# Performance work log

Measured on AMD Instinct MI355X. Metric: run time of the kernel, lower is better.

## Reference

```python
import jax, jax.numpy as jnp
import numpy as np

B, S_IMG, S_TXT = 2, 2048, 256
DIM, H, D = 1024, 16, 64
EPS = 1e-6


def _rmsnorm(x, w):
    x32 = x.astype(jnp.float32)
    rms = jnp.sqrt(jnp.mean(x32 * x32, axis=-1, keepdims=True) + EPS)
    return (x32 / rms * w.astype(jnp.float32)).astype(x.dtype)


def _heads(x):  # [B,S,DIM] -> [B,H,S,D]
    b, s, _ = x.shape
    return x.reshape(b, s, H, D).transpose(0, 2, 1, 3)


def setup_inputs() -> dict:
    key = jax.random.key(0)
    ks = jax.random.split(key, 20)
    lin = lambda k: (jax.random.normal(k, (DIM, DIM), jnp.float32) * 0.02,
                     jnp.zeros((DIM,), jnp.float32))
    wq, bq = lin(ks[0]); wk, bk = lin(ks[1]); wv, bv = lin(ks[2])
    waq, baq = lin(ks[3]); wak, bak = lin(ks[4]); wav, bav = lin(ks[5])
    wout, bout = lin(ks[6]); waout, baout = lin(ks[7])
    return {
        "img_hidden": jax.random.normal(ks[8], (B, S_IMG, DIM), jnp.float32),
        "txt_hidden": jax.random.normal(ks[9], (B, S_TXT, DIM), jnp.float32),
        "wq": wq, "bq": bq, "wk": wk, "bk": bk, "wv": wv, "bv": bv,
        "waq": waq, "baq": baq, "wak": wak, "bak": bak, "wav": wav, "bav": bav,
        "wout": wout, "bout": bout, "waout": waout, "baout": baout,
        "gq": jnp.ones((D,), jnp.float32), "gk": jnp.ones((D,), jnp.float32),
        "gaq": jnp.ones((D,), jnp.float32), "gak": jnp.ones((D,), jnp.float32),
    }


def reference(img_hidden, txt_hidden, wq, bq, wk, bk, wv, bv,
              waq, baq, wak, bak, wav, bav, wout, bout, waout, baout,
              gq, gk, gaq, gak):
    batch = img_hidden.shape[0]
    # joint QKV projections (torch Linear: x @ W.T + b)
    q = _heads(img_hidden @ wq.T + bq)
    k = _heads(img_hidden @ wk.T + bk)
    v = _heads(img_hidden @ wv.T + bv)
    aq = _heads(txt_hidden @ waq.T + baq)
    ak = _heads(txt_hidden @ wak.T + bak)
    av = _heads(txt_hidden @ wav.T + bav)
    # per-head RMSNorm on Q/K
    q, k = _rmsnorm(q, gq), _rmsnorm(k, gk)
    aq, ak = _rmsnorm(aq, gaq), _rmsnorm(ak, gak)
    # concat streams along sequence: [B,H,S_img+S_txt,D]
    fq = jnp.concatenate([q, aq], axis=2)
    fk = jnp.concatenate([k, ak], axis=2)
    fv = jnp.concatenate([v, av], axis=2)
    scale = 1.0 / jnp.sqrt(jnp.float32(D))
    attn = jnp.einsum('bhqd,bhkd->bhqk', fq, fk) * scale
    attn = jax.nn.softmax(attn, axis=-1)
    out = jnp.einsum('bhqk,bhkd->bhqd', attn, fv)
    out = out.transpose(0, 2, 1, 3)  # [B,S,H,D]
    s_img = q.shape[2]
    img_out = out[:, :s_img].reshape(batch, s_img, -1)
    txt_out = out[:, s_img:].reshape(batch, aq.shape[2], -1)
    img_out = img_out @ wout.T + bout
    txt_out = txt_out @ waout.T + baout
    return (img_out, txt_out)
```

## Files before the change

kernel.cpp:

```cpp
#include <hip/hip_runtime.h>
#include <stdint.h>

#define BATCH 2
#define SIMG 2048
#define STXT 256
#define STOT 2304
#define DIM 1024
#define NH 16
#define HD 64

typedef unsigned short u16;
typedef __attribute__((ext_vector_type(8))) short bf16x8;
typedef __attribute__((ext_vector_type(4))) float f32x4;

__device__ __forceinline__ u16 f2bf(float f) {
  union { float f; uint32_t u; } v; v.f = f;
  uint32_t r = (v.u + 0x7FFFu + ((v.u >> 16) & 1u)) >> 16;
  return (u16)r;
}
__device__ __forceinline__ float bf2f(u16 h) {
  union { uint32_t u; float f; } v; v.u = ((uint32_t)h) << 16; return v.f;
}

__device__ __forceinline__ void async_load16(const u16* g, u16* l) {
  __builtin_amdgcn_global_load_lds(
      (const __attribute__((address_space(1))) uint32_t*)g,
      (__attribute__((address_space(3))) uint32_t*)l, 16, 0, 0);
}

__device__ __forceinline__ bf16x8 cvt8(const float* p) {
  const f32x4 a = *(const f32x4*)p;
  const f32x4 b = *(const f32x4*)(p + 4);
  union { bf16x8 v; u16 s[8]; } r;
  r.s[0] = f2bf(a[0]); r.s[1] = f2bf(a[1]); r.s[2] = f2bf(a[2]); r.s[3] = f2bf(a[3]);
  r.s[4] = f2bf(b[0]); r.s[5] = f2bf(b[1]); r.s[6] = f2bf(b[2]); r.s[7] = f2bf(b[3]);
  return r.v;
}

__device__ __forceinline__ float gain_at(const u16* g, int d) {
  if (g[0] == 0) return ((const float*)g)[d];
  return bf2f(g[d]);
}

__global__ __launch_bounds__(256)
void cvt_all(const float* s0, const float* s1, const float* s2, const float* s3,
             const float* s4, const float* s5, const float* s6, const float* s7,
             const float* s8, const float* s9,
             u16* d0, u16* d1, u16* d2, u16* d3, u16* d4,
             u16* d5, u16* d6, u16* d7, u16* d8, u16* d9)
{
  const int z = blockIdx.z;
  const float* srcs[10] = {s0,s1,s2,s3,s4,s5,s6,s7,s8,s9};
  u16* dsts[10] = {d0,d1,d2,d3,d4,d5,d6,d7,d8,d9};
  const int ns[10] = {BATCH*SIMG*DIM, BATCH*STXT*DIM, DIM*DIM, DIM*DIM, DIM*DIM,
                      DIM*DIM, DIM*DIM, DIM*DIM, DIM*DIM, DIM*DIM};
  const long i = ((long)blockIdx.x * 256 + threadIdx.x) * 8;
  if (i >= ns[z]) return;
  *(bf16x8*)(dsts[z] + i) = cvt8(srcs[z] + i);
}

template<int MODE>
__global__ __launch_bounds__(256)
void gemm_bt(const u16* __restrict__ Ai, const u16* __restrict__ At,
             const u16* __restrict__ Wi0, const u16* __restrict__ Wi1, const u16* __restrict__ Wi2,
             const u16* __restrict__ Wt0, const u16* __restrict__ Wt1, const u16* __restrict__ Wt2,
             const float* __restrict__ bi0, const float* __restrict__ bi1, const float* __restrict__ bi2,
             const float* __restrict__ bt0, const float* __restrict__ bt1, const float* __restrict__ bt2,
             void* __restrict__ Di0, void* __restrict__ Di1, void* __restrict__ Di2,
             void* __restrict__ Dt0, void* __restrict__ Dt1, void* __restrict__ Dt2,
             const u16* __restrict__ gi0, const u16* __restrict__ gi1,
             const u16* __restrict__ gt0, const u16* __restrict__ gt1,
             int ysplit)
{
  const int z = blockIdx.z;
  const bool txt = (int)blockIdx.y >= ysplit;
  const int yy = txt ? ((int)blockIdx.y - ysplit) : (int)blockIdx.y;

  const u16* A = txt ? At : Ai;
  const u16* W      = txt ? ((z == 0) ? Wt0 : ((z == 1) ? Wt1 : Wt2))
                          : ((z == 0) ? Wi0 : ((z == 1) ? Wi1 : Wi2));
  const float* bias = txt ? ((z == 0) ? bt0 : ((z == 1) ? bt1 : bt2))
                          : ((z == 0) ? bi0 : ((z == 1) ? bi1 : bi2));
  void* Dst         = txt ? ((z == 0) ? Dt0 : ((z == 1) ? Dt1 : Dt2))
                          : ((z == 0) ? Di0 : ((z == 1) ? Di1 : Di2));

  const int slog = txt ? 8 : 11;
  const int smask = (1 << slog) - 1;
  const int batch_rows = (MODE == 0) ? (txt ? STXT : SIMG) : STOT;
  const int src_off    = (MODE == 0) ? 0 : (txt ? SIMG : 0);
  const int dst_off    = (MODE == 0) ? (txt ? SIMG : 0) : 0;

  const int m0 = yy * 128;
  const int n0 = blockIdx.x * 128;
  const int tid = threadIdx.x;
  const int lane = tid & 63;
  const int w = tid >> 6;
  const int wm = w >> 1, wn = w & 1;
  const int l15 = lane & 15, quad = lane >> 4;

  __shared__ __attribute__((aligned(16))) u16 As[128 * 32];
  __shared__ __attribute__((aligned(16))) u16 Bs[128 * 32];

  const int srow = tid >> 2;
  const int scol = (tid & 3) * 8;

  long aoff0, aoff1;
  {
    int m = m0 + srow;
    aoff0 = ((long)(m >> slog) * batch_rows + src_off + (m & smask)) * DIM + scol;
    m = m0 + 64 + srow;
    aoff1 = ((long)(m >> slog) * batch_rows + src_off + (m & smask)) * DIM + scol;
  }
  const u16* wp0 = W + (long)(n0 + srow) * DIM + scol;
  const u16* wp1 = W + (long)(n0 + 64 + srow) * DIM + scol;
  u16* as0 = As + tid * 8;
  u16* as1 = As + 2048 + tid * 8;
  u16* bs0 = Bs + tid * 8;
  u16* bs1 = Bs + 2048 + tid * 8;

  const f32x4 fzero = {0.f, 0.f, 0.f, 0.f};
  f32x4 acc[4][4];
  #pragma unroll
  for (int i = 0; i < 4; ++i)
    #pragma unroll
    for (int j = 0; j < 4; ++j) acc[i][j] = fzero;

  for (int kt = 0; kt < DIM; kt += 32) {
    __syncthreads();
    async_load16(A + aoff0 + kt, as0);
    async_load16(A + aoff1 + kt, as1);
    async_load16(wp0 + kt, bs0);
    async_load16(wp1 + kt, bs1);
    __syncthreads();

    bf16x8 af[4], bfg[4];
    #pragma unroll
    for (int mt = 0; mt < 4; ++mt)
      af[mt] = *(const bf16x8*)(As + (wm * 64 + mt * 16 + l15) * 32 + quad * 8);
    #pragma unroll
    for (int nt = 0; nt < 4; ++nt)
      bfg[nt] = *(const bf16x8*)(Bs + (wn * 64 + nt * 16 + l15) * 32 + quad * 8);
    #pragma unroll
    for (int mt = 0; mt < 4; ++mt)
      #pragma unroll
      for (int nt = 0; nt < 4; ++nt)
        acc[mt][nt] = __builtin_amdgcn_mfma_f32_16x16x32_bf16(af[mt], bfg[nt], acc[mt][nt], 0, 0, 0);
  }

  if (MODE == 0 && z != 2) {
    const u16* gsel = txt ? ((z == 0) ? gt0 : gt1) : ((z == 0) ? gi0 : gi1);
    float gv[4];
    #pragma unroll
    for (int nt = 0; nt < 4; ++nt) gv[nt] = gain_at(gsel, nt * 16 + l15);
    #pragma unroll
    for (int mt = 0; mt < 4; ++mt) {
      float vals[4][4];
      #pragma unroll
      for (int nt = 0; nt < 4; ++nt) {
        const float bb = bias[n0 + wn * 64 + nt * 16 + l15];
        #pragma unroll
        for (int r = 0; r < 4; ++r) vals[nt][r] = acc[mt][nt][r] + bb;
      }
      #pragma unroll
      for (int r = 0; r < 4; ++r) {
        float ss = vals[0][r] * vals[0][r] + vals[1][r] * vals[1][r]
                 + vals[2][r] * vals[2][r] + vals[3][r] * vals[3][r];
        #pragma unroll
        for (int d = 1; d < 16; d <<= 1) ss += __shfl_xor(ss, d, 64);
        const float scn = rsqrtf(ss * (1.0f / 64.0f) + 1e-6f);
        const int grow = m0 + wm * 64 + mt * 16 + quad * 4 + r;
        const int b = grow >> slog;
        const int sl = grow & smask;
        #pragma unroll
        for (int nt = 0; nt < 4; ++nt) {
          const int gcol = n0 + wn * 64 + nt * 16 + l15;
          const int h = gcol >> 6, d2 = gcol & 63;
          const long idx = (((long)(b * NH + h)) * STOT + dst_off + sl) * HD + d2;
          ((u16*)Dst)[idx] = f2bf(vals[nt][r] * scn * gv[nt]);
        }
      }
    }
  } else {
    #pragma unroll
    for (int mt = 0; mt < 4; ++mt) {
      #pragma unroll
      for (int nt = 0; nt < 4; ++nt) {
        const int gcol = n0 + wn * 64 + nt * 16 + l15;
        const float bb = bias[gcol];
        const f32x4 v = acc[mt][nt];
        #pragma unroll
        for (int r = 0; r < 4; ++r) {
          const int grow = m0 + wm * 64 + mt * 16 + quad * 4 + r;
          const float val = v[r] + bb;
          if (MODE == 0) {
            const int b = grow >> slog;
            const int sl = grow & smask;
            const int h = gcol >> 6, d = gcol & 63;
            const long idx = (((long)(b * NH + h)) * HD + d) * STOT + dst_off + sl;
            ((u16*)Dst)[idx] = f2bf(val);
          } else {
            ((float*)Dst)[(long)grow * DIM + gcol] = val;
          }
        }
      }
    }
  }
}

__global__ __launch_bounds__(256)
void flash_attn(const u16* __restrict__ fq, const u16* __restrict__ fk,
                const u16* __restrict__ fvT, u16* __restrict__ aout)
{
  const int qt = blockIdx.x;
  const int bh = blockIdx.y;
  const int tid = threadIdx.x;
  const int lane = tid & 63;
  const int w = tid >> 6;
  const int l15 = lane & 15, quad = lane >> 4;
  const int x7 = l15 & 7;
  const long base = (long)bh * STOT * HD;
  const int b = bh >> 4, h = bh & 15;

  __shared__ __attribute__((aligned(16))) u16 Ks[64 * 64];
  __shared__ __attribute__((aligned(16))) u16 Vt[64 * 64];
  __shared__ __attribute__((aligned(16))) u16 Ps[64 * 72];

  bf16x8 aq[2];
  #pragma unroll
  for (int ks = 0; ks < 2; ++ks)
    aq[ks] = *(const bf16x8*)(fq + base +
        (long)(qt * 64 + w * 16 + l15) * 64 + ks * 32 + quad * 8);

  const f32x4 fzero = {0.f, 0.f, 0.f, 0.f};
  f32x4 Oc[4];
  float lsum[4];
  #pragma unroll
  for (int r = 0; r < 4; ++r) lsum[r] = 0.f;
  #pragma unroll
  for (int nt = 0; nt < 4; ++nt) Oc[nt] = fzero;

  const float C1 = 0.18033688011112042f;
  const float C8 = 11.541560327111707f;

  const int srow = tid >> 3;
  const int sseg = (tid & 7) ^ (srow & 7);
  const int sr2 = srow + 32;

  for (int it = 0; it < STOT / 64; ++it) {
    __syncthreads();
    const u16* ksrc = fk + base + (long)it * 64 * 64;
    async_load16(ksrc + srow * 64 + sseg * 8, Ks + tid * 8);
    async_load16(ksrc + sr2 * 64 + sseg * 8, Ks + 2048 + tid * 8);
    const u16* vsrc = fvT + base + (long)it * 64;
    async_load16(vsrc + (long)srow * STOT + sseg * 8, Vt + tid * 8);
    async_load16(vsrc + (long)sr2 * STOT + sseg * 8, Vt + 2048 + tid * 8);
    __syncthreads();

    f32x4 sc[4];
    #pragma unroll
    for (int nt = 0; nt < 4; ++nt) sc[nt] = fzero;
    #pragma unroll
    for (int ks = 0; ks < 2; ++ks) {
      bf16x8 bk[4];
      #pragma unroll
      for (int nt = 0; nt < 4; ++nt)
        bk[nt] = *(const bf16x8*)(Ks + (nt * 16 + l15) * 64 + (((ks * 4 + quad) ^ x7) * 8));
      #pragma unroll
      for (int nt = 0; nt < 4; ++nt)
        sc[nt] = __builtin_amdgcn_mfma_f32_16x16x32_bf16(aq[ks], bk[nt], sc[nt], 0, 0, 0);
    }

    #pragma unroll
    for (int r = 0; r < 4; ++r) {
      const int prow = (w * 16 + quad * 4 + r) * 72;
      float ls = 0.f;
      #pragma unroll
      for (int nt = 0; nt < 4; ++nt) {
        const float p = exp2f(sc[nt][r] * C1 - C8);
        const uint32_t u = __float_as_uint(p);
        Ps[prow + nt * 16 + l15] = (u16)(u >> 16);
        ls += __uint_as_float(u & 0xFFFF0000u);
      }
      lsum[r] += ls;
    }

    #pragma unroll
    for (int ks = 0; ks < 2; ++ks) {
      const bf16x8 ap = *(const bf16x8*)(Ps + (w * 16 + l15) * 72 + ks * 32 + quad * 8);
      bf16x8 bv[4];
      #pragma unroll
      for (int nt = 0; nt < 4; ++nt)
        bv[nt] = *(const bf16x8*)(Vt + (nt * 16 + l15) * 64 + (((ks * 4 + quad) ^ x7) * 8));
      #pragma unroll
      for (int nt = 0; nt < 4; ++nt)
        Oc[nt] = __builtin_amdgcn_mfma_f32_16x16x32_bf16(ap, bv[nt], Oc[nt], 0, 0, 0);
    }
  }

  float inv[4];
  #pragma unroll
  for (int r = 0; r < 4; ++r) {
    float ls = lsum[r];
    #pragma unroll
    for (int d = 1; d < 16; d <<= 1) ls += __shfl_xor(ls, d, 64);
    inv[r] = 1.0f / ls;
  }

  #pragma unroll
  for (int nt = 0; nt < 4; ++nt) {
    const int d = nt * 16 + l15;
    #pragma unroll
    for (int r = 0; r < 4; ++r) {
      const int q = qt * 64 + w * 16 + quad * 4 + r;
      aout[(((long)b * STOT + q) * NH + h) * HD + d] = f2bf(Oc[nt][r] * inv[r]);
    }
  }
}

extern "C" void kernel_launch(void* const* d_in, const int* in_sizes, int n_in,
                              void* d_out, int out_size, void* d_ws, size_t ws_size,
                              hipStream_t stream)
{
  int iImg = 0, iTxt = 1;
  if (in_sizes[0] < in_sizes[1]) { iImg = 1; iTxt = 0; }
  const float* img  = (const float*)d_in[iImg];
  const float* txt  = (const float*)d_in[iTxt];
  const float* wq   = (const float*)d_in[2];
  const float* bq   = (const float*)d_in[3];
  const float* wk   = (const float*)d_in[4];
  const float* bk   = (const float*)d_in[5];
  const float* wv   = (const float*)d_in[6];
  const float* bv   = (const float*)d_in[7];
  const float* waq  = (const float*)d_in[8];
  const float* baq  = (const float*)d_in[9];
  const float* wak  = (const float*)d_in[10];
  const float* bak  = (const float*)d_in[11];
  const float* wav  = (const float*)d_in[12];
  const float* bav  = (const float*)d_in[13];
  const float* wout = (const float*)d_in[14];
  const float* bout = (const float*)d_in[15];
  const float* waout= (const float*)d_in[16];
  const float* baout= (const float*)d_in[17];
  const u16* gq   = (const u16*)d_in[18];
  const u16* gk   = (const u16*)d_in[19];
  const u16* gaq  = (const u16*)d_in[20];
  const u16* gak  = (const u16*)d_in[21];

  const long NE = (long)BATCH * NH * STOT * HD;
  const long NIMG = (long)BATCH * SIMG * DIM;
  const long NW = (long)DIM * DIM;

  u16* fq  = (u16*)d_ws;
  u16* fk  = fq + NE;
  u16* fvT = fk + NE;
  u16* imgb = fvT + NE;
  u16* txtb = imgb + NIMG;
  u16* aob  = imgb;
  u16* woutb  = imgb + NE;
  u16* waoutb = woutb + NW;
  u16* qw = (u16*)d_out;
  u16* wqb = qw, *wkb = qw + NW, *wvb = qw + 2*NW;
  u16* waqb = qw + 3*NW, *wakb = qw + 4*NW, *wavb = qw + 5*NW;
  float* out = (float*)d_out;
  float* outt = out + (long)BATCH * SIMG * DIM;

  const dim3 blk(256, 1, 1);

  hipLaunchKernelGGL(cvt_all, dim3((int)(NIMG / 2048), 1, 10), blk, 0, stream,
                     img, txt, wq, wk, wv, waq, wak, wav, wout, waout,
                     imgb, txtb, wqb, wkb, wvb, waqb, wakb, wavb, woutb, waoutb);
  hipLaunchKernelGGL((gemm_bt<0>), dim3(8, 36, 3), blk, 0, stream,
                     imgb, txtb, wqb, wkb, wvb, waqb, wakb, wavb,
                     bq, bk, bv, baq, bak, bav,
                     fq, fk, fvT, fq, fk, fvT,
                     gq, gk, gaq, gak, 32);
  hipLaunchKernelGGL(flash_attn, dim3(STOT / 64, BATCH * NH), blk, 0, stream,
                     fq, fk, fvT, aob);
  hipLaunchKernelGGL((gemm_bt<1>), dim3(8, 36, 1), blk, 0, stream,
                     aob, aob, woutb, woutb, woutb, waoutb, waoutb, waoutb,
                     bout, bout, bout, baout, baout, baout,
                     out, out, out, outt, outt, outt,
                     nullptr, nullptr, nullptr, nullptr, 32);
}
```

Measured before the change: 315.5 us.

## Split attention KV range across two blocks and combine partials in separate kernel

Splits the flash attention key/value loop into two halves handled by separate blocks along a new grid dimension. Each writes unnormalized bf16 partial outputs and row sums, and a new combine kernel sums them and normalizes. This aims to raise parallelism and shorten per-block serial work, at the cost of an extra kernel launch, extra memory traffic and bf16 rounding of partial outputs.

```diff
diff --git a/kernel.cpp b/kernel.cpp
--- a/kernel.cpp
+++ b/kernel.cpp
@@ -208,11 +208,18 @@
 }
 
 __global__ __launch_bounds__(256)
-void flash_attn(const u16* __restrict__ fq, const u16* __restrict__ fk,
-                const u16* __restrict__ fvT, u16* __restrict__ aout)
+void flash_attn_split(const u16* __restrict__ fq, const u16* __restrict__ fk,
+                      const u16* __restrict__ fvT,
+                      u16* __restrict__ p0, u16* __restrict__ p1,
+                      float* __restrict__ l0, float* __restrict__ l1)
 {
   const int qt = blockIdx.x;
   const int bh = blockIdx.y;
+  const int z = blockIdx.z;
+  u16* pout = z ? p1 : p0;
+  float* lout = z ? l1 : l0;
+  const int it0 = z * (STOT / 128);
+
   const int tid = threadIdx.x;
   const int lane = tid & 63;
   const int w = tid >> 6;
@@ -246,7 +253,7 @@
   const int sseg = (tid & 7) ^ (srow & 7);
   const int sr2 = srow + 32;
 
-  for (int it = 0; it < STOT / 64; ++it) {
+  for (int it = it0; it < it0 + STOT / 128; ++it) {
     __syncthreads();
     const u16* ksrc = fk + base + (long)it * 64 * 64;
     async_load16(ksrc + srow * 64 + sseg * 8, Ks + tid * 8);
@@ -297,13 +304,13 @@
     }
   }
 
-  float inv[4];
   #pragma unroll
   for (int r = 0; r < 4; ++r) {
     float ls = lsum[r];
     #pragma unroll
     for (int d = 1; d < 16; d <<= 1) ls += __shfl_xor(ls, d, 64);
-    inv[r] = 1.0f / ls;
+    if (l15 == 0)
+      lout[(long)bh * STOT + qt * 64 + w * 16 + quad * 4 + r] = ls;
   }
 
   #pragma unroll
@@ -312,9 +319,30 @@
     #pragma unroll
     for (int r = 0; r < 4; ++r) {
       const int q = qt * 64 + w * 16 + quad * 4 + r;
-      aout[(((long)b * STOT + q) * NH + h) * HD + d] = f2bf(Oc[nt][r] * inv[r]);
-    }
-  }
+      pout[(((long)b * STOT + q) * NH + h) * HD + d] = f2bf(Oc[nt][r]);
+    }
+  }
+}
+
+__global__ __launch_bounds__(256)
+void attn_combine(const u16* __restrict__ p1, const float* __restrict__ l0,
+                  const float* __restrict__ l1, u16* __restrict__ p0io)
+{
+  const long i = ((long)blockIdx.x * 256 + threadIdx.x) * 8;
+  const long rem = i >> 6;
+  const int h = (int)(rem & 15);
+  const long bq = rem >> 4;
+  const int b = bq >= STOT;
+  const int q = (int)(bq - (long)b * STOT);
+  const long li = ((long)(b * NH + h)) * STOT + q;
+  const float inv = 1.0f / (l0[li] + l1[li]);
+  union { bf16x8 v; u16 s[8]; } a, c, o;
+  a.v = *(const bf16x8*)(p0io + i);
+  c.v = *(const bf16x8*)(p1 + i);
+  #pragma unroll
+  for (int j = 0; j < 8; ++j)
+    o.s[j] = f2bf((bf2f(a.s[j]) + bf2f(c.s[j])) * inv);
+  *(bf16x8*)(p0io + i) = o.v;
 }
 
 extern "C" void kernel_launch(void* const* d_in, const int* in_sizes, int n_in,
@@ -358,9 +386,12 @@
   u16* aob  = imgb;
   u16* woutb  = imgb + NE;
   u16* waoutb = woutb + NW;
+  float* lsum0 = (float*)(waoutb + NW);
+  float* lsum1 = lsum0 + (long)BATCH * NH * STOT;
   u16* qw = (u16*)d_out;
   u16* wqb = qw, *wkb = qw + NW, *wvb = qw + 2*NW;
   u16* waqb = qw + 3*NW, *wakb = qw + 4*NW, *wavb = qw + 5*NW;
+  u16* p1 = (u16*)d_out;
   float* out = (float*)d_out;
   float* outt = out + (long)BATCH * SIMG * DIM;
 
@@ -374,8 +405,10 @@
                      bq, bk, bv, baq, bak, bav,
                      fq, fk, fvT, fq, fk, fvT,
                      gq, gk, gaq, gak, 32);
-  hipLaunchKernelGGL(flash_attn, dim3(STOT / 64, BATCH * NH), blk, 0, stream,
-                     fq, fk, fvT, aob);
+  hipLaunchKernelGGL(flash_attn_split, dim3(STOT / 64, BATCH * NH, 2), blk, 0, stream,
+                     fq, fk, fvT, aob, p1, lsum0, lsum1);
+  hipLaunchKernelGGL(attn_combine, dim3((int)(NE / 2048)), blk, 0, stream,
+                     p1, lsum0, lsum1, aob);
   hipLaunchKernelGGL((gemm_bt<1>), dim3(8, 36, 1), blk, 0, stream,
                      aob, aob, woutb, woutb, woutb, waoutb, waoutb, waoutb,
                      bout, bout, bout, baout, baout, baout,
```

New measurement: 308.5 us. -2.2%, faster.
